# Kernel optimization log

Measured on AMD Instinct MI355X. Metric: run time of the kernel, lower is better.

## Reference

```python
import jax, jax.numpy as jnp
import numpy as np

BLOCK_SIZE = 64
N_EMBD = 128
N_HEAD = 4
HEAD_DIM = N_EMBD // N_HEAD  # 32


def setup_inputs() -> dict:
    key = jax.random.key(0)
    kx, kq, kk, kv = jax.random.split(key, 4)
    B, T = 4096, 64
    x = jax.random.normal(kx, (B, T, N_EMBD), dtype=jnp.float32)
    # nn.Linear(n_embd, head_dim, bias=False): stored as [out,in] in torch,
    # here kept as [in, out] = [128, 32] so projection is x @ W.
    s = 1.0 / np.sqrt(N_EMBD)
    Wq = jax.random.uniform(kq, (N_EMBD, HEAD_DIM), jnp.float32, -s, s)
    Wk = jax.random.uniform(kk, (N_EMBD, HEAD_DIM), jnp.float32, -s, s)
    Wv = jax.random.uniform(kv, (N_EMBD, HEAD_DIM), jnp.float32, -s, s)
    return {"x": x, "Wq": Wq, "Wk": Wk, "Wv": Wv}


def reference(x, Wq, Wk, Wv):
    B, T, C = x.shape
    q = x @ Wq  # [B, T, Hd]
    k = x @ Wk
    v = x @ Wv
    scale = 1.0 / jnp.sqrt(jnp.asarray(k.shape[-1], x.dtype))
    wei = jnp.einsum("btd,bsd->bts", q, k) * scale  # [B, T, T]
    causal = jnp.tril(jnp.ones((T, T), dtype=bool))
    wei = jnp.where(causal, wei, -jnp.inf)
    wei = jax.nn.softmax(wei, axis=-1)
    out = jnp.einsum("bts,bsd->btd", wei, v)  # [B, T, Hd]
    return out
```

## Files before the change

### kernel.cpp

```cpp
#include <hip/hip_runtime.h>


#define TT 64
#define CC 128
#define HD 32

typedef __bf16 bf16_t;
typedef __bf16 bf8_t __attribute__((ext_vector_type(8)));
typedef __bf16 bf4_t __attribute__((ext_vector_type(4)));
typedef float  f4_t  __attribute__((ext_vector_type(4)));

__global__ __launch_bounds__(256) void prep_weights(
    const float* __restrict__ Wq, const float* __restrict__ Wk,
    const float* __restrict__ Wv, bf16_t* __restrict__ wf)
{
  int t = blockIdx.x * 256 + threadIdx.x;
  int j    = t & 7;
  int lane = (t >> 3) & 63;
  int kt   = (t >> 9) & 3;
  int n6   = t >> 11;
  int k    = kt * 32 + (lane >> 4) * 8 + j;
  int col  = (n6 & 1) * 16 + (lane & 15);
  const float* W = (n6 >> 1) == 0 ? Wq : ((n6 >> 1) == 1 ? Wk : Wv);
  float v = W[k * HD + col];
  if (n6 < 2) v *= 0.17677669529663687f;
  wf[t] = (bf16_t)v;
}

__global__ __launch_bounds__(64, 2) void head_fused(
    const float* __restrict__ x, const bf8_t* __restrict__ wf,
    float* __restrict__ out)
{
  __shared__ __align__(16) bf16_t qs[TT][40];
  __shared__ __align__(16) bf16_t ks[TT][40];
  __shared__ __align__(16) bf16_t vt[HD][72];
  __shared__ __align__(16) bf16_t ps[16][72];

  const int lane = threadIdx.x;
  const int quad = lane >> 4;
  const int l16  = lane & 15;
  const int b    = blockIdx.x;
  const float* __restrict__ xblk = x + (size_t)b * (TT * CC);
  float* __restrict__ ob = out + (size_t)b * (TT * HD);

  const f4_t zero4 = {0.f, 0.f, 0.f, 0.f};
  bf8_t ones8;
  #pragma unroll
  for (int t = 0; t < 8; ++t) ones8[t] = (bf16_t)1.0f;

  bf8_t wfr[24];
  float4 ta[8], tb[8];

  auto load_tile = [&](float4* d, int i) {
    #pragma unroll
    for (int kk = 0; kk < 4; ++kk) {
      const float* s = xblk + (16 * i + l16) * CC + kk * 32 + quad * 8;
      d[2 * kk]     = *(const float4*)s;
      d[2 * kk + 1] = *(const float4*)(s + 4);
    }
  };

  auto proj_tile = [&](const float4* d, int i) {
    f4_t acc[6];
    #pragma unroll
    for (int n = 0; n < 6; ++n) acc[n] = zero4;
    #pragma unroll
    for (int kk = 0; kk < 4; ++kk) {
      float4 f0 = d[2 * kk], f1 = d[2 * kk + 1];
      bf8_t a;
      a[0] = (bf16_t)f0.x; a[1] = (bf16_t)f0.y; a[2] = (bf16_t)f0.z; a[3] = (bf16_t)f0.w;
      a[4] = (bf16_t)f1.x; a[5] = (bf16_t)f1.y; a[6] = (bf16_t)f1.z; a[7] = (bf16_t)f1.w;
      #pragma unroll
      for (int n = 0; n < 6; ++n)
        acc[n] = __builtin_amdgcn_mfma_f32_16x16x32_bf16(a, wfr[n * 4 + kk], acc[n], 0, 0, 0);
    }
    #pragma unroll
    for (int r = 0; r < 4; ++r) {
      int row = 16 * i + quad * 4 + r;
      qs[row][l16]      = (bf16_t)acc[0][r];
      qs[row][16 + l16] = (bf16_t)acc[1][r];
      ks[row][l16]      = (bf16_t)acc[2][r];
      ks[row][16 + l16] = (bf16_t)acc[3][r];
    }
    bf4_t v0 = { (bf16_t)acc[4][0], (bf16_t)acc[4][1], (bf16_t)acc[4][2], (bf16_t)acc[4][3] };
    bf4_t v1 = { (bf16_t)acc[5][0], (bf16_t)acc[5][1], (bf16_t)acc[5][2], (bf16_t)acc[5][3] };
    *(bf4_t*)&vt[l16][16 * i + quad * 4]      = v0;
    *(bf4_t*)&vt[16 + l16][16 * i + quad * 4] = v1;
  };

  auto sm_tile = [&](int i) {
    f4_t sc[4];
    bf8_t aq = *(const bf8_t*)&qs[16 * i + l16][quad * 8];
    #pragma unroll
    for (int j = 0; j < 4; ++j) {
      sc[j] = zero4;
      if (j <= i) {
        bf8_t bk = *(const bf8_t*)&ks[16 * j + l16][quad * 8];
        sc[j] = __builtin_amdgcn_mfma_f32_16x16x32_bf16(aq, bk, zero4, 0, 0, 0);
      }
    }
    #pragma unroll
    for (int r = 0; r < 4; ++r) {
      int rl = quad * 4 + r;
      #pragma unroll
      for (int j = 0; j < 4; ++j) {
        if (j <= i) {
          bool valid = (j < i) | (l16 <= rl);
          float e = __expf(sc[j][r]);
          ps[rl][j * 16 + l16] = (bf16_t)(valid ? e : 0.f);
        } else if (j == (i | 1)) {
          ps[rl][j * 16 + l16] = (bf16_t)0.f;
        }
      }
    }
    f4_t o0 = zero4, o1 = zero4, osum = zero4;
    #pragma unroll
    for (int kk = 0; kk <= (i >> 1); ++kk) {
      int k0 = kk * 32 + quad * 8;
      bf8_t ap  = *(const bf8_t*)&ps[l16][k0];
      bf8_t bv0 = *(const bf8_t*)&vt[l16][k0];
      bf8_t bv1 = *(const bf8_t*)&vt[16 + l16][k0];
      o0   = __builtin_amdgcn_mfma_f32_16x16x32_bf16(ap, bv0, o0, 0, 0, 0);
      o1   = __builtin_amdgcn_mfma_f32_16x16x32_bf16(ap, bv1, o1, 0, 0, 0);
      osum = __builtin_amdgcn_mfma_f32_16x16x32_bf16(ap, ones8, osum, 0, 0, 0);
    }
    #pragma unroll
    for (int r = 0; r < 4; ++r) {
      int row = 16 * i + quad * 4 + r;
      float inv = __builtin_amdgcn_rcpf(osum[r]);
      ob[row * HD + l16]      = o0[r] * inv;
      ob[row * HD + 16 + l16] = o1[r] * inv;
    }
  };

  load_tile(ta, 0);
  #pragma unroll
  for (int t = 0; t < 24; ++t) wfr[t] = wf[t * 64 + lane];
  load_tile(tb, 1);
  proj_tile(ta, 0);  load_tile(ta, 2);
  proj_tile(tb, 1);  load_tile(tb, 3);
  proj_tile(ta, 2);
  sm_tile(0);
  sm_tile(1);
  proj_tile(tb, 3);
  sm_tile(2);
  sm_tile(3);
}

extern "C" void kernel_launch(void* const* d_in, const int* in_sizes, int n_in,
                              void* d_out, int out_size, void* d_ws, size_t ws_size,
                              hipStream_t stream) {
  const float* x  = (const float*)d_in[0];
  const float* Wq = (const float*)d_in[1];
  const float* Wk = (const float*)d_in[2];
  const float* Wv = (const float*)d_in[3];
  float* out = (float*)d_out;
  bf16_t* wf = (bf16_t*)d_ws;
  int B = in_sizes[0] / (TT * CC);

  prep_weights<<<dim3(48), dim3(256), 0, stream>>>(Wq, Wk, Wv, wf);
  head_fused<<<dim3(B), dim3(64), 0, stream>>>(x, (const bf8_t*)wf, out);
}
```

Baseline: 206.3 us.

## Stream weights per k-slice and drop Q smem to raise occupancy to 3 waves

Instead of holding all 24 weight fragments and two x tiles in registers, the kernel now streams weights from global memory per k-slice through double-buffered register sets and loads the next x tile in halves inside the projection loop. The Q shared buffer is removed: each Q tile is staged through ps and read back into registers (aq[4]). Launch bounds go from 2 to 3 waves per SIMD. The aim is to cut register and LDS pressure so more waves can hide latency, at the cost of re-reading weights from global/L2 for every tile and moving all projections ahead of softmax, which loses the earlier overlap.

Result: slower. 221.6 us (+7.4%).

```diff
diff --git a/kernel.cpp b/kernel.cpp
--- a/kernel.cpp
+++ b/kernel.cpp
@@ -27,11 +27,10 @@
   wf[t] = (bf16_t)v;
 }
 
-__global__ __launch_bounds__(64, 2) void head_fused(
+__global__ __launch_bounds__(64, 3) void head_fused(
     const float* __restrict__ x, const bf8_t* __restrict__ wf,
     float* __restrict__ out)
 {
-  __shared__ __align__(16) bf16_t qs[TT][40];
   __shared__ __align__(16) bf16_t ks[TT][40];
   __shared__ __align__(16) bf16_t vt[HD][72];
   __shared__ __align__(16) bf16_t ps[16][72];
@@ -44,41 +43,64 @@
   float* __restrict__ ob = out + (size_t)b * (TT * HD);
 
   const f4_t zero4 = {0.f, 0.f, 0.f, 0.f};
-  bf8_t ones8;
-  #pragma unroll
-  for (int t = 0; t < 8; ++t) ones8[t] = (bf16_t)1.0f;
 
-  bf8_t wfr[24];
-  float4 ta[8], tb[8];
+  bf8_t wA[6], wB[6];
+  bf8_t aq[4];
+  float4 tf[8];
 
-  auto load_tile = [&](float4* d, int i) {
+  auto wload = [&](bf8_t* w, int kkn) {
     #pragma unroll
-    for (int kk = 0; kk < 4; ++kk) {
+    for (int n = 0; n < 6; ++n) w[n] = wf[(n * 4 + kkn) * 64 + lane];
+  };
+  auto load_half = [&](int i, int h) {
+    #pragma unroll
+    for (int kk = 2 * h; kk < 2 * h + 2; ++kk) {
       const float* s = xblk + (16 * i + l16) * CC + kk * 32 + quad * 8;
-      d[2 * kk]     = *(const float4*)s;
-      d[2 * kk + 1] = *(const float4*)(s + 4);
+      tf[2 * kk]     = *(const float4*)s;
+      tf[2 * kk + 1] = *(const float4*)(s + 4);
     }
   };
+  auto cvt8 = [&](int kk) -> bf8_t {
+    float4 f0 = tf[2 * kk], f1 = tf[2 * kk + 1];
+    bf8_t a;
+    a[0] = (bf16_t)f0.x; a[1] = (bf16_t)f0.y; a[2] = (bf16_t)f0.z; a[3] = (bf16_t)f0.w;
+    a[4] = (bf16_t)f1.x; a[5] = (bf16_t)f1.y; a[6] = (bf16_t)f1.z; a[7] = (bf16_t)f1.w;
+    return a;
+  };
 
-  auto proj_tile = [&](const float4* d, int i) {
+  auto proj_tile = [&](int i, int inext) {
     f4_t acc[6];
     #pragma unroll
     for (int n = 0; n < 6; ++n) acc[n] = zero4;
+    bf8_t a;
+    wload(wB, 1);
+    a = cvt8(0);
     #pragma unroll
-    for (int kk = 0; kk < 4; ++kk) {
-      float4 f0 = d[2 * kk], f1 = d[2 * kk + 1];
-      bf8_t a;
-      a[0] = (bf16_t)f0.x; a[1] = (bf16_t)f0.y; a[2] = (bf16_t)f0.z; a[3] = (bf16_t)f0.w;
-      a[4] = (bf16_t)f1.x; a[5] = (bf16_t)f1.y; a[6] = (bf16_t)f1.z; a[7] = (bf16_t)f1.w;
-      #pragma unroll
-      for (int n = 0; n < 6; ++n)
-        acc[n] = __builtin_amdgcn_mfma_f32_16x16x32_bf16(a, wfr[n * 4 + kk], acc[n], 0, 0, 0);
-    }
+    for (int n = 0; n < 6; ++n)
+      acc[n] = __builtin_amdgcn_mfma_f32_16x16x32_bf16(a, wA[n], acc[n], 0, 0, 0);
+    wload(wA, 2);
+    a = cvt8(1);
+    #pragma unroll
+    for (int n = 0; n < 6; ++n)
+      acc[n] = __builtin_amdgcn_mfma_f32_16x16x32_bf16(a, wB[n], acc[n], 0, 0, 0);
+    if (inext < 4) load_half(inext, 0);
+    wload(wB, 3);
+    a = cvt8(2);
+    #pragma unroll
+    for (int n = 0; n < 6; ++n)
+      acc[n] = __builtin_amdgcn_mfma_f32_16x16x32_bf16(a, wA[n], acc[n], 0, 0, 0);
+    wload(wA, 0);
+    a = cvt8(3);
+    if (inext < 4) load_half(inext, 1);
+    #pragma unroll
+    for (int n = 0; n < 6; ++n)
+      acc[n] = __builtin_amdgcn_mfma_f32_16x16x32_bf16(a, wB[n], acc[n], 0, 0, 0);
     #pragma unroll
     for (int r = 0; r < 4; ++r) {
-      int row = 16 * i + quad * 4 + r;
-      qs[row][l16]      = (bf16_t)acc[0][r];
-      qs[row][16 + l16] = (bf16_t)acc[1][r];
+      int rl  = quad * 4 + r;
+      int row = 16 * i + rl;
+      ps[rl][l16]       = (bf16_t)acc[0][r];
+      ps[rl][16 + l16]  = (bf16_t)acc[1][r];
       ks[row][l16]      = (bf16_t)acc[2][r];
       ks[row][16 + l16] = (bf16_t)acc[3][r];
     }
@@ -86,17 +108,22 @@
     bf4_t v1 = { (bf16_t)acc[5][0], (bf16_t)acc[5][1], (bf16_t)acc[5][2], (bf16_t)acc[5][3] };
     *(bf4_t*)&vt[l16][16 * i + quad * 4]      = v0;
     *(bf4_t*)&vt[16 + l16][16 * i + quad * 4] = v1;
+    aq[i] = *(const bf8_t*)&ps[l16][quad * 8];
   };
+
+  bf8_t ones8;
+  #pragma unroll
+  for (int t = 0; t < 8; ++t) ones8[t] = (bf16_t)1.0f;
 
   auto sm_tile = [&](int i) {
     f4_t sc[4];
-    bf8_t aq = *(const bf8_t*)&qs[16 * i + l16][quad * 8];
+    bf8_t aqv = aq[i];
     #pragma unroll
     for (int j = 0; j < 4; ++j) {
       sc[j] = zero4;
       if (j <= i) {
         bf8_t bk = *(const bf8_t*)&ks[16 * j + l16][quad * 8];
-        sc[j] = __builtin_amdgcn_mfma_f32_16x16x32_bf16(aq, bk, zero4, 0, 0, 0);
+        sc[j] = __builtin_amdgcn_mfma_f32_16x16x32_bf16(aqv, bk, zero4, 0, 0, 0);
       }
     }
     #pragma unroll
@@ -133,16 +160,14 @@
     }
   };
 
-  load_tile(ta, 0);
-  #pragma unroll
-  for (int t = 0; t < 24; ++t) wfr[t] = wf[t * 64 + lane];
-  load_tile(tb, 1);
-  proj_tile(ta, 0);  load_tile(ta, 2);
-  proj_tile(tb, 1);  load_tile(tb, 3);
-  proj_tile(ta, 2);
+  load_half(0, 0); load_half(0, 1);
+  wload(wA, 0);
+  proj_tile(0, 1);
+  proj_tile(1, 2);
+  proj_tile(2, 3);
+  proj_tile(3, 4);
   sm_tile(0);
   sm_tile(1);
-  proj_tile(tb, 3);
   sm_tile(2);
   sm_tile(3);
 }
```

## Stream x in per-chunk prefetches instead of double-buffered whole tiles

Applied to the files above, without the earlier changes.

Replaces the two whole-tile register buffers for x with a single 32-column chunk buffer that is prefetched one chunk ahead inside the projection loop. All four projection tiles now run before the softmax/attention tiles instead of interleaving the last projection with attention. This cuts register pressure from the large float4 buffers, at the cost of a much shallower load-ahead distance that may expose global memory latency.

Result: no change. 208.9 us (+1.2%).

```diff
diff --git a/kernel.cpp b/kernel.cpp
--- a/kernel.cpp
+++ b/kernel.cpp
@@ -44,35 +44,35 @@
   float* __restrict__ ob = out + (size_t)b * (TT * HD);
 
   const f4_t zero4 = {0.f, 0.f, 0.f, 0.f};
-  bf8_t ones8;
-  #pragma unroll
-  for (int t = 0; t < 8; ++t) ones8[t] = (bf16_t)1.0f;
 
   bf8_t wfr[24];
-  float4 ta[8], tb[8];
+  float4 qf[2];
 
-  auto load_tile = [&](float4* d, int i) {
-    #pragma unroll
-    for (int kk = 0; kk < 4; ++kk) {
-      const float* s = xblk + (16 * i + l16) * CC + kk * 32 + quad * 8;
-      d[2 * kk]     = *(const float4*)s;
-      d[2 * kk + 1] = *(const float4*)(s + 4);
-    }
+  auto load_q = [&](int i, int p) {
+    const float* s = xblk + (16 * i + l16) * CC + p * 32 + quad * 8;
+    qf[0] = *(const float4*)s;
+    qf[1] = *(const float4*)(s + 4);
+  };
+  auto cvtq = [&]() -> bf8_t {
+    float4 f0 = qf[0], f1 = qf[1];
+    bf8_t a;
+    a[0] = (bf16_t)f0.x; a[1] = (bf16_t)f0.y; a[2] = (bf16_t)f0.z; a[3] = (bf16_t)f0.w;
+    a[4] = (bf16_t)f1.x; a[5] = (bf16_t)f1.y; a[6] = (bf16_t)f1.z; a[7] = (bf16_t)f1.w;
+    return a;
   };
 
-  auto proj_tile = [&](const float4* d, int i) {
+  auto proj_tile = [&](int i) {
     f4_t acc[6];
     #pragma unroll
     for (int n = 0; n < 6; ++n) acc[n] = zero4;
     #pragma unroll
-    for (int kk = 0; kk < 4; ++kk) {
-      float4 f0 = d[2 * kk], f1 = d[2 * kk + 1];
-      bf8_t a;
-      a[0] = (bf16_t)f0.x; a[1] = (bf16_t)f0.y; a[2] = (bf16_t)f0.z; a[3] = (bf16_t)f0.w;
-      a[4] = (bf16_t)f1.x; a[5] = (bf16_t)f1.y; a[6] = (bf16_t)f1.z; a[7] = (bf16_t)f1.w;
+    for (int p = 0; p < 4; ++p) {
+      bf8_t a = cvtq();
+      if (p < 3)      load_q(i, p + 1);
+      else if (i < 3) load_q(i + 1, 0);
       #pragma unroll
       for (int n = 0; n < 6; ++n)
-        acc[n] = __builtin_amdgcn_mfma_f32_16x16x32_bf16(a, wfr[n * 4 + kk], acc[n], 0, 0, 0);
+        acc[n] = __builtin_amdgcn_mfma_f32_16x16x32_bf16(a, wfr[n * 4 + p], acc[n], 0, 0, 0);
     }
     #pragma unroll
     for (int r = 0; r < 4; ++r) {
@@ -87,6 +87,10 @@
     *(bf4_t*)&vt[l16][16 * i + quad * 4]      = v0;
     *(bf4_t*)&vt[16 + l16][16 * i + quad * 4] = v1;
   };
+
+  bf8_t ones8;
+  #pragma unroll
+  for (int t = 0; t < 8; ++t) ones8[t] = (bf16_t)1.0f;
 
   auto sm_tile = [&](int i) {
     f4_t sc[4];
@@ -133,16 +137,15 @@
     }
   };
 
-  load_tile(ta, 0);
+  load_q(0, 0);
   #pragma unroll
   for (int t = 0; t < 24; ++t) wfr[t] = wf[t * 64 + lane];
-  load_tile(tb, 1);
-  proj_tile(ta, 0);  load_tile(ta, 2);
-  proj_tile(tb, 1);  load_tile(tb, 3);
-  proj_tile(ta, 2);
+  proj_tile(0);
+  proj_tile(1);
+  proj_tile(2);
+  proj_tile(3);
   sm_tile(0);
   sm_tile(1);
-  proj_tile(tb, 3);
   sm_tile(2);
   sm_tile(3);
 }
```
